# Optimization experiments

Hardware: AMD Instinct MI355X
Metric: run time of the kernel (lower is better)

Reference implementation:

```python
import jax, jax.numpy as jnp
import numpy as np

EPS = 1e-8
DIV_CONST = 512.0  # hardcoded in the original forward (np.dot(arange, 512))


def setup_inputs() -> dict:
    key = jax.random.key(0)
    k1, = jax.random.split(key, 1)
    B, C, T = 16, 512, 8192
    x = jax.random.normal(k1, (B, C, T), dtype=jnp.float32)
    gains = jnp.ones((1, C, 1), dtype=jnp.float32)
    bias = jnp.zeros((1, C, 1), dtype=jnp.float32)
    return {"x": x, "gains": gains, "bias": bias}


def reference(x, gains, bias):
    # x: [B, C, T]
    B, C, T = x.shape
    divid = jnp.arange(1, T + 1, dtype=x.dtype) * DIV_CONST  # [T]
    # cumulative (causal) channel+time mean and second moment
    mean = jnp.cumsum(x.sum(axis=1), axis=1) / divid          # [B, T]
    mean_sq = jnp.cumsum((x * x).sum(axis=1), axis=1) / divid # [B, T]
    var = mean_sq - mean * mean                               # [B, T]
    xn = (x - mean[:, None, :]) * jax.lax.rsqrt(var[:, None, :] + EPS)
    return xn * gains + bias
```

## Files before the change

kernel.cpp:

```cpp
#include <hip/hip_runtime.h>
#include <math.h>

#define B_  16
#define C_  512
#define T_  8192
#define T4_ (T_/4)

__global__ void sums_kernel(const float* __restrict__ x,
                            float* __restrict__ partial,
                            int c_per_chunk, int nchunk) {
    int t4 = blockIdx.x * blockDim.x + threadIdx.x;
    int b = blockIdx.y;
    int chunk = blockIdx.z;
    const float4* xb = (const float4*)x + ((size_t)(b * C_ + chunk * c_per_chunk)) * T4_;
    float4 s  = make_float4(0.f, 0.f, 0.f, 0.f);
    float4 ss = make_float4(0.f, 0.f, 0.f, 0.f);
    #pragma unroll 8
    for (int c = 0; c < c_per_chunk; ++c) {
        float4 v = xb[(size_t)c * T4_ + t4];
        s.x += v.x;       s.y += v.y;       s.z += v.z;       s.w += v.w;
        ss.x += v.x * v.x; ss.y += v.y * v.y; ss.z += v.z * v.z; ss.w += v.w * v.w;
    }
    size_t base = (size_t)(b * nchunk + chunk) * 2 * T4_;
    ((float4*)partial)[base + t4]        = s;
    ((float4*)partial)[base + T4_ + t4]  = ss;
}

__global__ void scan_kernel(const float* __restrict__ partial,
                            float* __restrict__ meano,
                            float* __restrict__ rstdo,
                            int nchunk) {
    const int b   = blockIdx.x;
    const int tid = threadIdx.x;
    const int PER = T_ / 256;
    const int t0  = tid * PER;

    float ls[32], lss[32];
    double tot_s = 0.0, tot_ss = 0.0;
    for (int i = 0; i < PER; ++i) {
        int t = t0 + i;
        float sv = 0.f, ssv = 0.f;
        for (int ch = 0; ch < nchunk; ++ch) {
            size_t base = (size_t)(b * nchunk + ch) * 2 * T_;
            sv  += partial[base + t];
            ssv += partial[base + T_ + t];
        }
        ls[i] = sv; lss[i] = ssv;
        tot_s += sv; tot_ss += ssv;
    }

    __shared__ double sh_s[256], sh_ss[256];
    sh_s[tid] = tot_s; sh_ss[tid] = tot_ss;
    __syncthreads();
    double pre_s = 0.0, pre_ss = 0.0;
    for (int j = 0; j < tid; ++j) { pre_s += sh_s[j]; pre_ss += sh_ss[j]; }

    double run_s = pre_s, run_ss = pre_ss;
    for (int i = 0; i < PER; ++i) {
        run_s  += (double)ls[i];
        run_ss += (double)lss[i];
        int t = t0 + i;
        double div = 512.0 * (double)(t + 1);
        double m   = run_s / div;
        double msq = run_ss / div;
        double var = msq - m * m;
        double r   = 1.0 / sqrt(var + 1e-8);
        meano[b * T_ + t] = (float)m;
        rstdo[b * T_ + t] = (float)r;
    }
}

__global__ void norm_kernel(const float* __restrict__ x,
                            const float* __restrict__ gains,
                            const float* __restrict__ bias,
                            const float* __restrict__ meanv,
                            const float* __restrict__ rstdv,
                            float* __restrict__ out) {
    int i  = blockIdx.x * blockDim.x + threadIdx.x;
    int t4 = i & (T4_ - 1);
    int bc = i >> 11;
    int c  = bc & (C_ - 1);
    int b  = bc >> 9;

    float4 xv = ((const float4*)x)[i];
    float4 mv = ((const float4*)meanv)[b * T4_ + t4];
    float4 rv = ((const float4*)rstdv)[b * T4_ + t4];
    float g  = gains[c];
    float bi = bias[c];

    float4 o;
    o.x = (xv.x - mv.x) * rv.x * g + bi;
    o.y = (xv.y - mv.y) * rv.y * g + bi;
    o.z = (xv.z - mv.z) * rv.z * g + bi;
    o.w = (xv.w - mv.w) * rv.w * g + bi;
    ((float4*)out)[i] = o;
}

extern "C" void kernel_launch(void* const* d_in, const int* in_sizes, int n_in,
                              void* d_out, int out_size, void* d_ws, size_t ws_size,
                              hipStream_t stream) {
    const float* x     = (const float*)d_in[0];
    const float* gains = (const float*)d_in[1];
    const float* bias  = (const float*)d_in[2];
    float* out = (float*)d_out;
    float* ws  = (float*)d_ws;

    const size_t BT = (size_t)B_ * T_;

    int nchunk = 8;
    while (nchunk > 1 &&
           ws_size < (2 * BT + (size_t)B_ * nchunk * 2 * T_) * sizeof(float)) {
        nchunk >>= 1;
    }
    float* meanv   = ws;
    float* rstdv   = ws + BT;
    float* partial = ws + 2 * BT;
    int c_per_chunk = C_ / nchunk;

    dim3 g1(T4_ / 256, B_, nchunk);
    sums_kernel<<<g1, 256, 0, stream>>>(x, partial, c_per_chunk, nchunk);

    scan_kernel<<<B_, 256, 0, stream>>>(partial, meanv, rstdv, nchunk);

    int total4 = B_ * C_ * T4_;
    norm_kernel<<<total4 / 256, 256, 0, stream>>>(x, gains, bias, meanv, rstdv, out);
}
```

Before: 575.5 us.

## Fuse sums, scan and normalize into one decoupled-lookback single-pass kernel

```diff
diff --git a/kernel.cpp b/kernel.cpp
--- a/kernel.cpp
+++ b/kernel.cpp
@@ -1,99 +1,190 @@
 #include <hip/hip_runtime.h>
 #include <math.h>
 
-#define B_  16
-#define C_  512
-#define T_  8192
-#define T4_ (T_/4)
-
-__global__ void sums_kernel(const float* __restrict__ x,
-                            float* __restrict__ partial,
-                            int c_per_chunk, int nchunk) {
-    int t4 = blockIdx.x * blockDim.x + threadIdx.x;
-    int b = blockIdx.y;
-    int chunk = blockIdx.z;
-    const float4* xb = (const float4*)x + ((size_t)(b * C_ + chunk * c_per_chunk)) * T4_;
+#define B_    16
+#define C_    512
+#define T_    8192
+#define T4_   (T_/4)
+#define TILE  32
+#define TF4   (TILE/4)
+#define NT_   (T_/TILE)
+#define NBLK  (B_*NT_)
+#define NTHR  512
+
+#define FLAG_AGG 1
+#define FLAG_INC 2
+
+__device__ __forceinline__ double wave_sum(double v) {
+    #pragma unroll
+    for (int m = 1; m < 64; m <<= 1) v += __shfl_xor(v, m, 64);
+    return v;
+}
+
+extern "C" __global__ void __launch_bounds__(NTHR, 4)
+fused_cumnorm(const float* __restrict__ x,
+              const float* __restrict__ gains,
+              const float* __restrict__ bias,
+              float* __restrict__ out,
+              int* __restrict__ flags,
+              unsigned int* __restrict__ ticket,
+              double* __restrict__ vals)
+{
+    __shared__ float4 red_s[8][8];
+    __shared__ float4 red_ss[8][8];
+    __shared__ float4 sh_mean[8];
+    __shared__ float4 sh_rstd[8];
+    __shared__ unsigned int sh_tk;
+
+    const int tid  = threadIdx.x;
+    const int lane = tid & 63;
+    const int wid  = tid >> 6;
+    const int t4   = lane & 7;
+    const int cg   = lane >> 3;
+
+    if (tid == 0) sh_tk = atomicAdd(ticket, 1u);
+    __syncthreads();
+    const int tk  = (int)sh_tk;
+    const int b   = tk & (B_ - 1);
+    const int j   = tk >> 4;
+    const int rec = b * NT_ + j;
+
+    const float4* x4 = (const float4*)x;
+    const size_t tcol  = (size_t)j * TF4 + t4;
+    const int    cbase = wid * 8 + cg;
+
+    float4 v[8];
     float4 s  = make_float4(0.f, 0.f, 0.f, 0.f);
     float4 ss = make_float4(0.f, 0.f, 0.f, 0.f);
-    #pragma unroll 8
-    for (int c = 0; c < c_per_chunk; ++c) {
-        float4 v = xb[(size_t)c * T4_ + t4];
-        s.x += v.x;       s.y += v.y;       s.z += v.z;       s.w += v.w;
-        ss.x += v.x * v.x; ss.y += v.y * v.y; ss.z += v.z * v.z; ss.w += v.w * v.w;
-    }
-    size_t base = (size_t)(b * nchunk + chunk) * 2 * T4_;
-    ((float4*)partial)[base + t4]        = s;
-    ((float4*)partial)[base + T4_ + t4]  = ss;
-}
-
-__global__ void scan_kernel(const float* __restrict__ partial,
-                            float* __restrict__ meano,
-                            float* __restrict__ rstdo,
-                            int nchunk) {
-    const int b   = blockIdx.x;
-    const int tid = threadIdx.x;
-    const int PER = T_ / 256;
-    const int t0  = tid * PER;
-
-    float ls[32], lss[32];
-    double tot_s = 0.0, tot_ss = 0.0;
-    for (int i = 0; i < PER; ++i) {
-        int t = t0 + i;
-        float sv = 0.f, ssv = 0.f;
-        for (int ch = 0; ch < nchunk; ++ch) {
-            size_t base = (size_t)(b * nchunk + ch) * 2 * T_;
-            sv  += partial[base + t];
-            ssv += partial[base + T_ + t];
-        }
-        ls[i] = sv; lss[i] = ssv;
-        tot_s += sv; tot_ss += ssv;
-    }
-
-    __shared__ double sh_s[256], sh_ss[256];
-    sh_s[tid] = tot_s; sh_ss[tid] = tot_ss;
+    #pragma unroll
+    for (int p = 0; p < 8; ++p) {
+        const int c = p * 64 + cbase;
+        float4 xv = x4[(size_t)(b * C_ + c) * T4_ + tcol];
+        v[p] = xv;
+        s.x += xv.x; s.y += xv.y; s.z += xv.z; s.w += xv.w;
+        ss.x += xv.x * xv.x; ss.y += xv.y * xv.y;
+        ss.z += xv.z * xv.z; ss.w += xv.w * xv.w;
+    }
+    #pragma unroll
+    for (int m = 8; m < 64; m <<= 1) {
+        s.x  += __shfl_xor(s.x,  m, 64); s.y  += __shfl_xor(s.y,  m, 64);
+        s.z  += __shfl_xor(s.z,  m, 64); s.w  += __shfl_xor(s.w,  m, 64);
+        ss.x += __shfl_xor(ss.x, m, 64); ss.y += __shfl_xor(ss.y, m, 64);
+        ss.z += __shfl_xor(ss.z, m, 64); ss.w += __shfl_xor(ss.w, m, 64);
+    }
+    if (lane < 8) { red_s[wid][t4] = s; red_ss[wid][t4] = ss; }
     __syncthreads();
-    double pre_s = 0.0, pre_ss = 0.0;
-    for (int j = 0; j < tid; ++j) { pre_s += sh_s[j]; pre_ss += sh_ss[j]; }
-
-    double run_s = pre_s, run_ss = pre_ss;
-    for (int i = 0; i < PER; ++i) {
-        run_s  += (double)ls[i];
-        run_ss += (double)lss[i];
-        int t = t0 + i;
-        double div = 512.0 * (double)(t + 1);
-        double m   = run_s / div;
-        double msq = run_ss / div;
-        double var = msq - m * m;
-        double r   = 1.0 / sqrt(var + 1e-8);
-        meano[b * T_ + t] = (float)m;
-        rstdo[b * T_ + t] = (float)r;
-    }
-}
-
-__global__ void norm_kernel(const float* __restrict__ x,
-                            const float* __restrict__ gains,
-                            const float* __restrict__ bias,
-                            const float* __restrict__ meanv,
-                            const float* __restrict__ rstdv,
-                            float* __restrict__ out) {
-    int i  = blockIdx.x * blockDim.x + threadIdx.x;
-    int t4 = i & (T4_ - 1);
-    int bc = i >> 11;
-    int c  = bc & (C_ - 1);
-    int b  = bc >> 9;
-
-    float4 xv = ((const float4*)x)[i];
-    float4 mv = ((const float4*)meanv)[b * T4_ + t4];
-    float4 rv = ((const float4*)rstdv)[b * T4_ + t4];
-    float g  = gains[c];
-    float bi = bias[c];
-
-    float4 o;
-    o.x = (xv.x - mv.x) * rv.x * g + bi;
-    o.y = (xv.y - mv.y) * rv.y * g + bi;
-    o.z = (xv.z - mv.z) * rv.z * g + bi;
-    o.w = (xv.w - mv.w) * rv.w * g + bi;
-    ((float4*)out)[i] = o;
+
+    if (wid == 0) {
+        float4 a  = red_s[cg][t4];
+        float4 aa = red_ss[cg][t4];
+        #pragma unroll
+        for (int m = 8; m < 64; m <<= 1) {
+            a.x  += __shfl_xor(a.x,  m, 64); a.y  += __shfl_xor(a.y,  m, 64);
+            a.z  += __shfl_xor(a.z,  m, 64); a.w  += __shfl_xor(a.w,  m, 64);
+            aa.x += __shfl_xor(aa.x, m, 64); aa.y += __shfl_xor(aa.y, m, 64);
+            aa.z += __shfl_xor(aa.z, m, 64); aa.w += __shfl_xor(aa.w, m, 64);
+        }
+        const double d0 = a.x,  d1 = d0 + a.y,  d2 = d1 + a.z,  d3 = d2 + a.w;
+        const double e0 = aa.x, e1 = e0 + aa.y, e2 = e1 + aa.z, e3 = e2 + aa.w;
+        double sc_s = d3, sc_ss = e3;
+        #pragma unroll
+        for (int off = 1; off < 8; off <<= 1) {
+            double u = __shfl_up(sc_s,  off, 64);
+            double w = __shfl_up(sc_ss, off, 64);
+            if (lane >= off) { sc_s += u; sc_ss += w; }
+        }
+        const double agg_s  = __shfl(sc_s,  7, 64);
+        const double agg_ss = __shfl(sc_ss, 7, 64);
+
+        if (lane == 0 && j > 0) {
+            __hip_atomic_store(&vals[0 * NBLK + rec], agg_s,  __ATOMIC_RELAXED, __HIP_MEMORY_SCOPE_AGENT);
+            __hip_atomic_store(&vals[1 * NBLK + rec], agg_ss, __ATOMIC_RELAXED, __HIP_MEMORY_SCOPE_AGENT);
+            __hip_atomic_store(&flags[rec], FLAG_AGG, __ATOMIC_RELEASE, __HIP_MEMORY_SCOPE_AGENT);
+        }
+
+        double ps = 0.0, pss = 0.0;
+        int hi = j - 1;
+        while (hi >= 0) {
+            const int p = hi - lane;
+            int f = 0;
+            if (p >= 0) {
+                const int fr = b * NT_ + p;
+                do {
+                    f = __hip_atomic_load(&flags[fr], __ATOMIC_ACQUIRE, __HIP_MEMORY_SCOPE_AGENT);
+                    if (f == 0) __builtin_amdgcn_s_sleep(2);
+                } while (f == 0);
+            }
+            const unsigned long long m2 = __ballot(p >= 0 && f == FLAG_INC);
+            const int stop = m2 ? (__ffsll((unsigned long long)m2) - 1) : 64;
+            double vs = 0.0, vss = 0.0;
+            if (p >= 0 && lane <= stop) {
+                const int fr = b * NT_ + p;
+                if (lane == stop) {
+                    vs  = __hip_atomic_load(&vals[2 * NBLK + fr], __ATOMIC_RELAXED, __HIP_MEMORY_SCOPE_AGENT);
+                    vss = __hip_atomic_load(&vals[3 * NBLK + fr], __ATOMIC_RELAXED, __HIP_MEMORY_SCOPE_AGENT);
+                } else {
+                    vs  = __hip_atomic_load(&vals[0 * NBLK + fr], __ATOMIC_RELAXED, __HIP_MEMORY_SCOPE_AGENT);
+                    vss = __hip_atomic_load(&vals[1 * NBLK + fr], __ATOMIC_RELAXED, __HIP_MEMORY_SCOPE_AGENT);
+                }
+            }
+            ps  += wave_sum(vs);
+            pss += wave_sum(vss);
+            if (m2) break;
+            hi -= 64;
+        }
+
+        if (lane == 0) {
+            __hip_atomic_store(&vals[2 * NBLK + rec], ps + agg_s,   __ATOMIC_RELAXED, __HIP_MEMORY_SCOPE_AGENT);
+            __hip_atomic_store(&vals[3 * NBLK + rec], pss + agg_ss, __ATOMIC_RELAXED, __HIP_MEMORY_SCOPE_AGENT);
+            __hip_atomic_store(&flags[rec], FLAG_INC, __ATOMIC_RELEASE, __HIP_MEMORY_SCOPE_AGENT);
+        }
+
+        if (lane < 8) {
+            const double ex_s  = ps  + (sc_s  - d3);
+            const double ex_ss = pss + (sc_ss - e3);
+            const int tg = j * TILE + t4 * 4;
+            float4 mv, rv;
+            {
+                const double div = 512.0 * (double)(tg + 1);
+                const double m = (ex_s + d0) / div, q = (ex_ss + e0) / div;
+                mv.x = (float)m; rv.x = (float)(1.0 / sqrt(q - m * m + 1e-8));
+            }
+            {
+                const double div = 512.0 * (double)(tg + 2);
+                const double m = (ex_s + d1) / div, q = (ex_ss + e1) / div;
+                mv.y = (float)m; rv.y = (float)(1.0 / sqrt(q - m * m + 1e-8));
+            }
+            {
+                const double div = 512.0 * (double)(tg + 3);
+                const double m = (ex_s + d2) / div, q = (ex_ss + e2) / div;
+                mv.z = (float)m; rv.z = (float)(1.0 / sqrt(q - m * m + 1e-8));
+            }
+            {
+                const double div = 512.0 * (double)(tg + 4);
+                const double m = (ex_s + d3) / div, q = (ex_ss + e3) / div;
+                mv.w = (float)m; rv.w = (float)(1.0 / sqrt(q - m * m + 1e-8));
+            }
+            sh_mean[t4] = mv; sh_rstd[t4] = rv;
+        }
+    }
+    __syncthreads();
+
+    const float4 mv = sh_mean[t4];
+    const float4 rv = sh_rstd[t4];
+    float4* o4 = (float4*)out;
+    #pragma unroll
+    for (int p = 0; p < 8; ++p) {
+        const int c = p * 64 + cbase;
+        const float g  = gains[c];
+        const float bi = bias[c];
+        const float4 xv = v[p];
+        float4 ov;
+        ov.x = (xv.x - mv.x) * rv.x * g + bi;
+        ov.y = (xv.y - mv.y) * rv.y * g + bi;
+        ov.z = (xv.z - mv.z) * rv.z * g + bi;
+        ov.w = (xv.w - mv.w) * rv.w * g + bi;
+        o4[(size_t)(b * C_ + c) * T4_ + tcol] = ov;
+    }
 }
 
 extern "C" void kernel_launch(void* const* d_in, const int* in_sizes, int n_in,
@@ -103,25 +194,14 @@
     const float* gains = (const float*)d_in[1];
     const float* bias  = (const float*)d_in[2];
     float* out = (float*)d_out;
-    float* ws  = (float*)d_ws;
-
-    const size_t BT = (size_t)B_ * T_;
-
-    int nchunk = 8;
-    while (nchunk > 1 &&
-           ws_size < (2 * BT + (size_t)B_ * nchunk * 2 * T_) * sizeof(float)) {
-        nchunk >>= 1;
-    }
-    float* meanv   = ws;
-    float* rstdv   = ws + BT;
-    float* partial = ws + 2 * BT;
-    int c_per_chunk = C_ / nchunk;
-
-    dim3 g1(T4_ / 256, B_, nchunk);
-    sums_kernel<<<g1, 256, 0, stream>>>(x, partial, c_per_chunk, nchunk);
-
-    scan_kernel<<<B_, 256, 0, stream>>>(partial, meanv, rstdv, nchunk);
-
-    int total4 = B_ * C_ * T4_;
-    norm_kernel<<<total4 / 256, 256, 0, stream>>>(x, gains, bias, meanv, rstdv, out);
+
+    char* ws = (char*)d_ws;
+    int* flags            = (int*)ws;
+    unsigned int* ticket  = (unsigned int*)(ws + NBLK * sizeof(int));
+    double* vals          = (double*)(ws + 32768);
+
+    hipMemsetAsync(d_ws, 0, NBLK * sizeof(int) + sizeof(unsigned int), stream);
+
+    fused_cumnorm<<<NBLK, NTHR, 0, stream>>>(x, gains, bias, out,
+                                             flags, ticket, vals);
 }
```

After: 873.3 us. +51.7%, slower.
